# Optimization experiments

Measured on AMD Instinct MI355X. Metric: run time of the kernel, lower is better.

## Reference

```python
import jax, jax.numpy as jnp
import numpy as np

M, N, D = 4, 65536, 256

def setup_inputs() -> dict:
    key = jax.random.key(0)
    k1, k2, k3 = jax.random.split(key, 3)
    x = jax.random.normal(k1, (M, N, D), dtype=jnp.float32)
    # W[i,j] is the (out,in) weight of fusion_layers[i][j]; b[i,j] its bias.
    W = jax.random.normal(k2, (M, M, D, D), dtype=jnp.float32) * (1.0 / np.sqrt(D))
    b = jax.random.normal(k3, (M, M, D), dtype=jnp.float32) * 0.02
    return {"x": x, "W": W, "b": b}

def reference(x, W, b):
    # x: [M, N, D] stacked modality features (zip(*features) rows vectorized over N)
    # out[i] = x[i] + sum_{j != i} (x[j] @ W[i,j]^T + b[i,j])
    m = x.shape[0]
    mask = (1.0 - jnp.eye(m)).astype(x.dtype)            # zero on diagonal (skip i==j)
    y = jnp.einsum('ijef,jnf->ijne', W, x) + b[:, :, None, :]  # [M, M, N, D]
    out = x + jnp.einsum('ij,ijne->ine', mask, y)         # fused masked accumulation
    return out
```

## Files before the change

### kernel.cpp

```cpp
#include <hip/hip_runtime.h>
#include <hip/hip_bf16.h>
#include <stdint.h>

#define NN 65536
#define DD 256

typedef uint32_t u32;
typedef __attribute__((ext_vector_type(4))) float f32x4;
typedef __attribute__((ext_vector_type(4))) u32 u32x4;
typedef __attribute__((ext_vector_type(2))) u32 u32x2;
typedef __attribute__((ext_vector_type(8))) short s16x8;

__device__ inline unsigned short f2bf(float f) {
    union { float f; u32 u; } v; v.f = f;
    u32 u = v.u;
    return (unsigned short)((u + 0x7fffu + ((u >> 16) & 1u)) >> 16);
}

__device__ inline float bf2f(unsigned short h) {
    union { u32 u; float f; } v; v.u = (u32)h << 16;
    return v.f;
}

__device__ inline void gl2lds16(const void* g, void* s) {
    __builtin_amdgcn_global_load_lds(
        (const __attribute__((address_space(1))) void*)g,
        (__attribute__((address_space(3))) void*)s, 16, 0, 0);
}

__global__ void prep_w256(const float* __restrict__ W, unsigned short* __restrict__ Wimg) {
    int t = blockIdx.x * blockDim.x + threadIdx.x;
    int E = t * 4;
    int tile = E >> 14;
    int pin = E & 16383;
    int col = pin >> 6;
    int r2e = pin & 63;
    int ct = tile >> 4;
    int j = (tile >> 2) & 3;
    int kk = tile & 3;
    int kl = r2e ^ ((col & 7) << 3);
    int i = ct;
    int e = col;
    int f = kk * 64 + kl;
    u32 p0, p1;
    if (i == j) {
        p0 = 0u; p1 = 0u;
    } else {
        f32x4 w = *(const f32x4*)(W + ((size_t)((i * 4 + j) * 256 + e) << 8) + f);
        p0 = (u32)f2bf(w[0]) | ((u32)f2bf(w[1]) << 16);
        p1 = (u32)f2bf(w[2]) | ((u32)f2bf(w[3]) << 16);
    }
    u32x2 pr = {p0, p1};
    *(u32x2*)(Wimg + E) = pr;
}

__global__ void prep_w128(const float* __restrict__ W, unsigned short* __restrict__ Wimg) {
    int t = blockIdx.x * blockDim.x + threadIdx.x;
    int E = t * 4;
    int tile = E >> 13;
    int pin = E & 8191;
    int col = pin >> 6;
    int r2e = pin & 63;
    int ct = tile >> 4;
    int j = (tile >> 2) & 3;
    int kk = tile & 3;
    int kl = r2e ^ ((col & 7) << 3);
    int c = ct * 128 + col;
    int i = c >> 8, e = c & 255;
    int f = kk * 64 + kl;
    u32 p0, p1;
    if (i == j) {
        p0 = 0u; p1 = 0u;
    } else {
        f32x4 w = *(const f32x4*)(W + ((size_t)((i * 4 + j) * 256 + e) << 8) + f);
        p0 = (u32)f2bf(w[0]) | ((u32)f2bf(w[1]) << 16);
        p1 = (u32)f2bf(w[2]) | ((u32)f2bf(w[3]) << 16);
    }
    u32x2 pr = {p0, p1};
    *(u32x2*)(Wimg + E) = pr;
}

__global__ void prep_x(const float* __restrict__ x, unsigned short* __restrict__ Ximg) {
    int t = blockIdx.x * blockDim.x + threadIdx.x;
    long long E = (long long)t * 4;
    int tile = (int)(E >> 14);
    int pin = (int)(E & 16383);
    int row = pin >> 6;
    int r2e = pin & 63;
    int kk = tile & 3;
    int rt = (tile >> 2) & 255;
    int j = tile >> 10;
    int kl = r2e ^ ((row & 7) << 3);
    int n = rt * 256 + row;
    int f = kk * 64 + kl;
    f32x4 v = *(const f32x4*)(x + ((size_t)j * NN + n) * DD + f);
    u32 p0 = (u32)f2bf(v[0]) | ((u32)f2bf(v[1]) << 16);
    u32 p1 = (u32)f2bf(v[2]) | ((u32)f2bf(v[3]) << 16);
    u32x2 pr = {p0, p1};
    *(u32x2*)(Ximg + E) = pr;
}

__global__ void prep_b(const float* __restrict__ b, float* __restrict__ bsum) {
    int c = blockIdx.x * blockDim.x + threadIdx.x;
    if (c >= 1024) return;
    int i = c >> 8, e = c & 255;
    float s = 0.0f;
    #pragma unroll
    for (int j = 0; j < 4; ++j)
        if (j != i) s += b[((i * 4 + j) << 8) + e];
    bsum[c] = s;
}

__global__ __launch_bounds__(512, 2) void fusion_gemm14(
    const unsigned short* __restrict__ Wimg, const unsigned short* __restrict__ Ximg,
    const float* __restrict__ bsum, float* __restrict__ out) {
    __shared__ __attribute__((aligned(16))) char lds[2][65536];

    const int tid = threadIdx.x;
    const int bid = blockIdx.x;
    const int xcd = bid & 7;
    const int slot = bid >> 3;
    const int ct = slot & 3;
    const int rhi = slot >> 2;
    const int rtile = rhi * 8 + xcd;
    const int n0 = rtile * 256;
    const int col0 = ct * 256;

    const int lane = tid & 63;
    const int wid = tid >> 6;
    const int wm = wid & 1;
    const int wn = wid >> 1;

    f32x4 acc[8][4];
    #pragma unroll
    for (int a = 0; a < 8; ++a)
        #pragma unroll
        for (int b2 = 0; b2 < 4; ++b2)
            acc[a][b2] = (f32x4){0.f, 0.f, 0.f, 0.f};

    const char* WimgB = (const char*)Wimg;
    const char* XimgB = (const char*)Ximg;
    const u32 loff = (u32)(wid * 1024);
    const u32 goff = (u32)(wid * 1024 + lane * 16);

    s16x8 fA0[2][4], fA1[2][4];
    s16x8 fB0[2][2], fB1[2][2];

#define STAGE_TILE(t_, D_)                                                            \
    {                                                                                 \
        int jj_ = (t_) >> 2;                                                          \
        int j_ = jj_ + (jj_ >= ct);                                                   \
        int kk_ = (t_) & 3;                                                           \
        const char* as_ = XimgB + (((size_t)((j_ * 256 + rtile) * 4 + kk_)) << 15) + goff; \
        const char* bs_ = WimgB + (((size_t)((ct * 4 + j_) * 4 + kk_)) << 15) + goff; \
        _Pragma("unroll")                                                             \
        for (int q = 0; q < 4; ++q) {                                                 \
            gl2lds16(as_ + q * 8192, (D_) + q * 8192 + loff);                         \
            gl2lds16(bs_ + q * 8192, (D_) + 32768 + q * 8192 + loff);                 \
        }                                                                             \
    }

#define RD_A(BUF_, mh_, SET_)                                                         \
    _Pragma("unroll")                                                                 \
    for (int kh = 0; kh < 2; ++kh) {                                                  \
        _Pragma("unroll")                                                             \
        for (int fm = 0; fm < 4; ++fm) {                                              \
            int r_ = wm * 128 + ((mh_) * 4 + fm) * 16 + (lane & 15);                  \
            u32 o_ = (u32)(r_ * 128 + kh * 64 + (lane >> 4) * 16);                    \
            o_ ^= (u32)((r_ & 7) << 4);                                               \
            SET_[kh][fm] = *(const s16x8*)((BUF_) + o_);                              \
        }                                                                             \
    }

#define RD_B(BUF_, nh_, SET_)                                                         \
    _Pragma("unroll")                                                                 \
    for (int kh = 0; kh < 2; ++kh) {                                                  \
        _Pragma("unroll")                                                             \
        for (int fn = 0; fn < 2; ++fn) {                                              \
            int c_ = wn * 64 + ((nh_) * 2 + fn) * 16 + (lane & 15);                   \
            u32 o_ = (u32)(c_ * 128 + kh * 64 + (lane >> 4) * 16);                    \
            o_ ^= (u32)((c_ & 7) << 4);                                               \
            SET_[kh][fn] = *(const s16x8*)((BUF_) + 32768 + o_);                      \
        }                                                                             \
    }

#define MM(AS_, BS_, mh_, nh_)                                                        \
    _Pragma("unroll")                                                                 \
    for (int kh = 0; kh < 2; ++kh) {                                                  \
        _Pragma("unroll")                                                             \
        for (int fm = 0; fm < 4; ++fm) {                                              \
            _Pragma("unroll")                                                         \
            for (int fn = 0; fn < 2; ++fn) {                                          \
                acc[(mh_) * 4 + fm][(nh_) * 2 + fn] =                                 \
                    __builtin_amdgcn_mfma_f32_16x16x32_bf16(                          \
                        AS_[kh][fm], BS_[kh][fn],                                     \
                        acc[(mh_) * 4 + fm][(nh_) * 2 + fn], 0, 0, 0);                \
            }                                                                         \
        }                                                                             \
    }

    STAGE_TILE(0, lds[0]);
    asm volatile("s_waitcnt vmcnt(0)" ::: "memory");
    __builtin_amdgcn_s_barrier();

    #pragma unroll 1
    for (int t = 0; t < 12; ++t) {
        const char* Bf = lds[t & 1];
        char* Of = lds[(t + 1) & 1];

        if (t < 11) STAGE_TILE(t + 1, Of);

        RD_A(Bf, 0, fA0);
        RD_B(Bf, 0, fB0);
        __builtin_amdgcn_s_setprio(1);
        MM(fA0, fB0, 0, 0);
        RD_B(Bf, 1, fB1);
        MM(fA0, fB1, 0, 1);
        RD_A(Bf, 1, fA1);
        MM(fA1, fB1, 1, 1);
        MM(fA1, fB0, 1, 0);
        __builtin_amdgcn_s_setprio(0);

        asm volatile("s_waitcnt vmcnt(0)" ::: "memory");
        __builtin_amdgcn_s_barrier();
    }

#undef STAGE_TILE
#undef RD_A
#undef RD_B
#undef MM

    {
        char* R = (char*)lds;
        #pragma unroll
        for (int kk = 0; kk < 4; ++kk) {
            const char* rs = XimgB + (((size_t)((ct * 256 + rtile) * 4 + kk)) << 15) + goff;
            #pragma unroll
            for (int q = 0; q < 4; ++q)
                gl2lds16(rs + q * 8192, R + kk * 32768 + q * 8192 + loff);
        }
        asm volatile("s_waitcnt vmcnt(0)" ::: "memory");
        __builtin_amdgcn_s_barrier();
    }

    const int r0 = (lane >> 4) * 4;
    const int cl = lane & 15;
    const char* Rb = (const char*)lds + (size_t)wn * 32768;
    #pragma unroll
    for (int mf = 0; mf < 8; ++mf) {
        #pragma unroll
        for (int nf = 0; nf < 4; ++nf) {
            int col_l = wn * 64 + nf * 16 + cl;
            float bs = bsum[col0 + col_l];
            #pragma unroll
            for (int r = 0; r < 4; ++r) {
                int row = wm * 128 + mf * 16 + r0 + r;
                int r2e = (nf * 16 + cl) ^ ((row & 7) << 3);
                float res = bf2f(*(const unsigned short*)(Rb + row * 128 + r2e * 2));
                int n = n0 + row;
                size_t oidx = ((size_t)ct * NN + n) * DD + col_l;
                out[oidx] = acc[mf][nf][r] + res + bs;
            }
        }
    }
}

__global__ __launch_bounds__(256, 2) void fusion_gemm_fb(
    const float* __restrict__ x, const unsigned short* __restrict__ Wimg,
    const float* __restrict__ bsum, float* __restrict__ out) {
    __shared__ __attribute__((aligned(16))) unsigned short Alds[128 * 64];
    __shared__ __attribute__((aligned(16))) unsigned short Blds[2][128 * 64];

    const int tid = threadIdx.x;
    const int bid = blockIdx.x;
    const int xcd = bid & 7;
    const int slot = bid >> 3;
    const int ct = slot & 7;
    const int rhi = slot >> 3;
    const int rtile = rhi * 8 + xcd;
    const int n0 = rtile * 128;
    const int col0 = ct * 128;
    const int i = ct >> 1;

    const int lane = tid & 63;
    const int wid = tid >> 6;
    const int wm = wid >> 1;
    const int wn = wid & 1;

    f32x4 acc[4][4];
    #pragma unroll
    for (int a = 0; a < 4; ++a)
        #pragma unroll
        for (int b2 = 0; b2 < 4; ++b2)
            acc[a][b2] = (f32x4){0.f, 0.f, 0.f, 0.f};

    const int sr = tid >> 1;
    const int sh = tid & 1;
    char* Ab = (char*)Alds;
    const char* WimgB = (const char*)Wimg;

    f32x4 av[8];
    {
        int j0 = (i == 0) ? 1 : 0;
        const float* asrc = x + (size_t)j0 * ((size_t)NN * DD) + (size_t)(n0 + sr) * DD + sh * 32;
        #pragma unroll
        for (int q = 0; q < 8; ++q) av[q] = *(const f32x4*)(asrc + q * 4);
        const char* base = WimgB + (((size_t)(ct * 4 + j0) * 4 + 0) << 14) + wid * 1024 + lane * 16;
        char* lb = (char*)Blds[0] + wid * 1024;
        #pragma unroll
        for (int q = 0; q < 4; ++q) gl2lds16(base + q * 4096, lb + q * 4096);
    }

    for (int t = 0; t < 12; ++t) {
        __syncthreads();
        #pragma unroll
        for (int q = 0; q < 4; ++q) {
            f32x4 v0 = av[2 * q], v1 = av[2 * q + 1];
            u32x4 p;
            p[0] = (u32)f2bf(v0[0]) | ((u32)f2bf(v0[1]) << 16);
            p[1] = (u32)f2bf(v0[2]) | ((u32)f2bf(v0[3]) << 16);
            p[2] = (u32)f2bf(v1[0]) | ((u32)f2bf(v1[1]) << 16);
            p[3] = (u32)f2bf(v1[2]) | ((u32)f2bf(v1[3]) << 16);
            u32 o = (u32)(sr * 128 + sh * 64 + q * 16);
            o ^= (u32)((sr & 7) << 4);
            *(u32x4*)(Ab + o) = p;
        }
        __syncthreads();

        if (t < 11) {
            int tn = t + 1;
            int jjn = tn >> 2;
            int jn = jjn + (jjn >= i);
            int kkn = tn & 3;
            const char* base = WimgB + (((size_t)(ct * 4 + jn) * 4 + kkn) << 14) + wid * 1024 + lane * 16;
            char* lb = (char*)Blds[tn & 1] + wid * 1024;
            #pragma unroll
            for (int q = 0; q < 4; ++q) gl2lds16(base + q * 4096, lb + q * 4096);
            const float* asrc = x + (size_t)jn * ((size_t)NN * DD) + (size_t)(n0 + sr) * DD + kkn * 64 + sh * 32;
            #pragma unroll
            for (int q = 0; q < 8; ++q) av[q] = *(const f32x4*)(asrc + q * 4);
        }

        const char* Bb = (const char*)Blds[t & 1];
        #pragma unroll
        for (int kh = 0; kh < 2; ++kh) {
            s16x8 af[4], bfr[4];
            #pragma unroll
            for (int fm = 0; fm < 4; ++fm) {
                int row = wm * 64 + fm * 16 + (lane & 15);
                u32 o = (u32)(row * 128 + kh * 64 + (lane >> 4) * 16);
                o ^= (u32)((row & 7) << 4);
                af[fm] = *(const s16x8*)(Ab + o);
            }
            #pragma unroll
            for (int fn = 0; fn < 4; ++fn) {
                int col = wn * 64 + fn * 16 + (lane & 15);
                u32 o = (u32)(col * 128 + kh * 64 + (lane >> 4) * 16);
                o ^= (u32)((col & 7) << 4);
                bfr[fn] = *(const s16x8*)(Bb + o);
            }
            #pragma unroll
            for (int fm = 0; fm < 4; ++fm)
                #pragma unroll
                for (int fn = 0; fn < 4; ++fn)
                    acc[fm][fn] = __builtin_amdgcn_mfma_f32_16x16x32_bf16(
                        af[fm], bfr[fn], acc[fm][fn], 0, 0, 0);
        }
    }

    const int r0 = (lane >> 4) * 4;
    const int cl = lane & 15;
    #pragma unroll
    for (int fm = 0; fm < 4; ++fm) {
        #pragma unroll
        for (int fn = 0; fn < 4; ++fn) {
            int col_l = wn * 64 + fn * 16 + cl;
            int cglob = col0 + col_l;
            float bs = bsum[cglob];
            int e = cglob & 255;
            #pragma unroll
            for (int r = 0; r < 4; ++r) {
                int row_l = wm * 64 + fm * 16 + r0 + r;
                int n = n0 + row_l;
                size_t oidx = ((size_t)i * NN + n) * DD + e;
                out[oidx] = acc[fm][fn][r] + x[oidx] + bs;
            }
        }
    }
}

extern "C" void kernel_launch(void* const* d_in, const int* in_sizes, int n_in,
                              void* d_out, int out_size, void* d_ws, size_t ws_size,
                              hipStream_t stream) {
    const float* x = (const float*)d_in[0];
    const float* W = (const float*)d_in[1];
    const float* b = (const float*)d_in[2];
    float* out = (float*)d_out;

    unsigned short* Wimg = (unsigned short*)d_ws;
    float* bsum = (float*)((char*)d_ws + ((size_t)8 << 20));
    const size_t ximg_off = (size_t)9 << 20;
    const size_t need = ximg_off + ((size_t)128 << 20);

    if (ws_size >= need) {
        unsigned short* Ximg = (unsigned short*)((char*)d_ws + ximg_off);
        hipLaunchKernelGGL(prep_b, dim3(4), dim3(256), 0, stream, b, bsum);
        hipLaunchKernelGGL(prep_w256, dim3(1024), dim3(256), 0, stream, W, Wimg);
        hipLaunchKernelGGL(prep_x, dim3(65536), dim3(256), 0, stream, x, Ximg);
        hipLaunchKernelGGL(fusion_gemm14, dim3(1024), dim3(512), 0, stream, Wimg, Ximg, bsum, out);
    } else {
        float* bsum2 = (float*)((char*)d_ws + ((size_t)2 << 20));
        hipLaunchKernelGGL(prep_b, dim3(4), dim3(256), 0, stream, b, bsum2);
        hipLaunchKernelGGL(prep_w128, dim3(1024), dim3(256), 0, stream, W, Wimg);
        hipLaunchKernelGGL(fusion_gemm_fb, dim3(4096), dim3(256), 0, stream, x, Wimg, bsum2, out);
    }
}
```

Baseline: 223.7 us.

## Drop X prepass; use producer/consumer warps converting fp32 X to bf16 in-kernel

Removes the separate prep_x pass that wrote a 128MB bf16 image of x. The main GEMM kernel now splits its warps: four producer warps load fp32 x, convert it to bf16 into swizzled LDS, and DMA weight tiles, while four consumer warps run the MFMA work. Output tiles shrink to 128 columns, so the grid doubles. The bias and weight prep kernels are merged into one launch. The aim is to cut global memory traffic and launch overhead, at the cost of halving the warps doing math and re-reading x for each column tile.

New measurement: 389.6 us. 74.2% more time.

```diff
diff --git a/kernel.cpp b/kernel.cpp
--- a/kernel.cpp
+++ b/kernel.cpp
@@ -28,108 +28,68 @@
         (__attribute__((address_space(3))) void*)s, 16, 0, 0);
 }
 
-__global__ void prep_w256(const float* __restrict__ W, unsigned short* __restrict__ Wimg) {
-    int t = blockIdx.x * blockDim.x + threadIdx.x;
-    int E = t * 4;
-    int tile = E >> 14;
-    int pin = E & 16383;
-    int col = pin >> 6;
-    int r2e = pin & 63;
-    int ct = tile >> 4;
-    int j = (tile >> 2) & 3;
-    int kk = tile & 3;
-    int kl = r2e ^ ((col & 7) << 3);
-    int i = ct;
-    int e = col;
-    int f = kk * 64 + kl;
-    u32 p0, p1;
-    if (i == j) {
-        p0 = 0u; p1 = 0u;
+__global__ void prep_small(const float* __restrict__ W, const float* __restrict__ b,
+                           unsigned short* __restrict__ Wimg, float* __restrict__ bsum) {
+    int bid = blockIdx.x;
+    if (bid < 1024) {
+        int t = bid * 256 + threadIdx.x;
+        int E = t * 4;
+        int tile = E >> 13;
+        int pin = E & 8191;
+        int col = pin >> 6;
+        int r2e = pin & 63;
+        int ct = tile >> 4;
+        int j = (tile >> 2) & 3;
+        int kk = tile & 3;
+        int kl = r2e ^ ((col & 7) << 3);
+        int c = ct * 128 + col;
+        int i = c >> 8, e = c & 255;
+        int f = kk * 64 + kl;
+        u32 p0, p1;
+        if (i == j) {
+            p0 = 0u; p1 = 0u;
+        } else {
+            f32x4 w = *(const f32x4*)(W + ((size_t)((i * 4 + j) * 256 + e) << 8) + f);
+            p0 = (u32)f2bf(w[0]) | ((u32)f2bf(w[1]) << 16);
+            p1 = (u32)f2bf(w[2]) | ((u32)f2bf(w[3]) << 16);
+        }
+        u32x2 pr = {p0, p1};
+        *(u32x2*)(Wimg + E) = pr;
     } else {
-        f32x4 w = *(const f32x4*)(W + ((size_t)((i * 4 + j) * 256 + e) << 8) + f);
-        p0 = (u32)f2bf(w[0]) | ((u32)f2bf(w[1]) << 16);
-        p1 = (u32)f2bf(w[2]) | ((u32)f2bf(w[3]) << 16);
-    }
-    u32x2 pr = {p0, p1};
-    *(u32x2*)(Wimg + E) = pr;
-}
-
-__global__ void prep_w128(const float* __restrict__ W, unsigned short* __restrict__ Wimg) {
-    int t = blockIdx.x * blockDim.x + threadIdx.x;
-    int E = t * 4;
-    int tile = E >> 13;
-    int pin = E & 8191;
-    int col = pin >> 6;
-    int r2e = pin & 63;
-    int ct = tile >> 4;
-    int j = (tile >> 2) & 3;
-    int kk = tile & 3;
-    int kl = r2e ^ ((col & 7) << 3);
-    int c = ct * 128 + col;
-    int i = c >> 8, e = c & 255;
-    int f = kk * 64 + kl;
-    u32 p0, p1;
-    if (i == j) {
-        p0 = 0u; p1 = 0u;
-    } else {
-        f32x4 w = *(const f32x4*)(W + ((size_t)((i * 4 + j) * 256 + e) << 8) + f);
-        p0 = (u32)f2bf(w[0]) | ((u32)f2bf(w[1]) << 16);
-        p1 = (u32)f2bf(w[2]) | ((u32)f2bf(w[3]) << 16);
-    }
-    u32x2 pr = {p0, p1};
-    *(u32x2*)(Wimg + E) = pr;
-}
-
-__global__ void prep_x(const float* __restrict__ x, unsigned short* __restrict__ Ximg) {
-    int t = blockIdx.x * blockDim.x + threadIdx.x;
-    long long E = (long long)t * 4;
-    int tile = (int)(E >> 14);
-    int pin = (int)(E & 16383);
-    int row = pin >> 6;
-    int r2e = pin & 63;
-    int kk = tile & 3;
-    int rt = (tile >> 2) & 255;
-    int j = tile >> 10;
-    int kl = r2e ^ ((row & 7) << 3);
-    int n = rt * 256 + row;
-    int f = kk * 64 + kl;
-    f32x4 v = *(const f32x4*)(x + ((size_t)j * NN + n) * DD + f);
-    u32 p0 = (u32)f2bf(v[0]) | ((u32)f2bf(v[1]) << 16);
-    u32 p1 = (u32)f2bf(v[2]) | ((u32)f2bf(v[3]) << 16);
-    u32x2 pr = {p0, p1};
-    *(u32x2*)(Ximg + E) = pr;
-}
-
-__global__ void prep_b(const float* __restrict__ b, float* __restrict__ bsum) {
-    int c = blockIdx.x * blockDim.x + threadIdx.x;
-    if (c >= 1024) return;
-    int i = c >> 8, e = c & 255;
-    float s = 0.0f;
-    #pragma unroll
-    for (int j = 0; j < 4; ++j)
-        if (j != i) s += b[((i * 4 + j) << 8) + e];
-    bsum[c] = s;
-}
-
-__global__ __launch_bounds__(512, 2) void fusion_gemm14(
-    const unsigned short* __restrict__ Wimg, const unsigned short* __restrict__ Ximg,
+        int c = (bid - 1024) * 256 + threadIdx.x;
+        if (c < 1024) {
+            int i = c >> 8, e = c & 255;
+            float s = 0.0f;
+            #pragma unroll
+            for (int j = 0; j < 4; ++j)
+                if (j != i) s += b[((i * 4 + j) << 8) + e];
+            bsum[c] = s;
+        }
+    }
+}
+
+__global__ __launch_bounds__(512, 2) void fusion_gemm17(
+    const float* __restrict__ x, const unsigned short* __restrict__ Wimg,
     const float* __restrict__ bsum, float* __restrict__ out) {
-    __shared__ __attribute__((aligned(16))) char lds[2][65536];
+    __shared__ __attribute__((aligned(16))) char lds[2][49152];
 
     const int tid = threadIdx.x;
     const int bid = blockIdx.x;
     const int xcd = bid & 7;
     const int slot = bid >> 3;
-    const int ct = slot & 3;
-    const int rhi = slot >> 2;
+    const int ct = slot & 7;
+    const int rhi = slot >> 3;
     const int rtile = rhi * 8 + xcd;
     const int n0 = rtile * 256;
-    const int col0 = ct * 256;
+    const int i = ct >> 1;
 
     const int lane = tid & 63;
     const int wid = tid >> 6;
+    const bool consumer = (wid < 4);
     const int wm = wid & 1;
-    const int wn = wid >> 1;
+    const int wn = (wid >> 1) & 1;
+    const int p = tid - 256;
+    const int pw = wid - 4;
 
     f32x4 acc[8][4];
     #pragma unroll
@@ -139,24 +99,39 @@
             acc[a][b2] = (f32x4){0.f, 0.f, 0.f, 0.f};
 
     const char* WimgB = (const char*)Wimg;
-    const char* XimgB = (const char*)Ximg;
-    const u32 loff = (u32)(wid * 1024);
-    const u32 goff = (u32)(wid * 1024 + lane * 16);
-
     s16x8 fA0[2][4], fA1[2][4];
     s16x8 fB0[2][2], fB1[2][2];
 
-#define STAGE_TILE(t_, D_)                                                            \
+#define P_LOAD(j_, kk_)                                                               \
     {                                                                                 \
-        int jj_ = (t_) >> 2;                                                          \
-        int j_ = jj_ + (jj_ >= ct);                                                   \
-        int kk_ = (t_) & 3;                                                           \
-        const char* as_ = XimgB + (((size_t)((j_ * 256 + rtile) * 4 + kk_)) << 15) + goff; \
-        const char* bs_ = WimgB + (((size_t)((ct * 4 + j_) * 4 + kk_)) << 15) + goff; \
-        _Pragma("unroll")                                                             \
-        for (int q = 0; q < 4; ++q) {                                                 \
-            gl2lds16(as_ + q * 8192, (D_) + q * 8192 + loff);                         \
-            gl2lds16(bs_ + q * 8192, (D_) + 32768 + q * 8192 + loff);                 \
+        const float* as_ = x + (size_t)(j_) * ((size_t)NN * DD)                       \
+                           + (size_t)(n0 + p) * DD + (kk_) * 64;                      \
+        _Pragma("unroll")                                                             \
+        for (int q = 0; q < 16; ++q) av[q] = *(const f32x4*)(as_ + q * 4);            \
+    }
+
+#define P_BDMA(j_, kk_, D_)                                                           \
+    {                                                                                 \
+        const char* bs_ = WimgB + (((size_t)((ct * 4 + (j_)) * 4 + (kk_))) << 14)     \
+                          + pw * 4096 + lane * 16;                                    \
+        _Pragma("unroll")                                                             \
+        for (int q = 0; q < 4; ++q)                                                   \
+            gl2lds16(bs_ + q * 1024, (D_) + 32768 + pw * 4096 + q * 1024);            \
+    }
+
+#define P_WRITE_A(D_)                                                                 \
+    {                                                                                 \
+        _Pragma("unroll")                                                             \
+        for (int q = 0; q < 8; ++q) {                                                 \
+            f32x4 v0 = av[2 * q], v1 = av[2 * q + 1];                                 \
+            u32x4 pk;                                                                 \
+            pk[0] = (u32)f2bf(v0[0]) | ((u32)f2bf(v0[1]) << 16);                      \
+            pk[1] = (u32)f2bf(v0[2]) | ((u32)f2bf(v0[3]) << 16);                      \
+            pk[2] = (u32)f2bf(v1[0]) | ((u32)f2bf(v1[1]) << 16);                      \
+            pk[3] = (u32)f2bf(v1[2]) | ((u32)f2bf(v1[3]) << 16);                      \
+            u32 o_ = (u32)(p * 128 + q * 16);                                         \
+            o_ ^= (u32)((p & 7) << 4);                                                \
+            *(u32x4*)((D_) + o_) = pk;                                                \
         }                                                                             \
     }
 
@@ -199,67 +174,91 @@
         }                                                                             \
     }
 
-    STAGE_TILE(0, lds[0]);
+    if (!consumer) {
+        f32x4 av[16];
+        int jj = 0, j0 = jj + (jj >= i);
+        P_LOAD(j0, 0);
+        P_BDMA(j0, 0, (char*)lds[0]);
+        P_WRITE_A((char*)lds[0]);
+    }
+    asm volatile("s_waitcnt lgkmcnt(0)" ::: "memory");
     asm volatile("s_waitcnt vmcnt(0)" ::: "memory");
     __builtin_amdgcn_s_barrier();
+    __builtin_amdgcn_sched_barrier(0);
 
     #pragma unroll 1
     for (int t = 0; t < 12; ++t) {
         const char* Bf = lds[t & 1];
         char* Of = lds[(t + 1) & 1];
 
-        if (t < 11) STAGE_TILE(t + 1, Of);
-
-        RD_A(Bf, 0, fA0);
-        RD_B(Bf, 0, fB0);
-        __builtin_amdgcn_s_setprio(1);
-        MM(fA0, fB0, 0, 0);
-        RD_B(Bf, 1, fB1);
-        MM(fA0, fB1, 0, 1);
-        RD_A(Bf, 1, fA1);
-        MM(fA1, fB1, 1, 1);
-        MM(fA1, fB0, 1, 0);
-        __builtin_amdgcn_s_setprio(0);
-
+        if (consumer) {
+            RD_A(Bf, 0, fA0);
+            RD_B(Bf, 0, fB0);
+            __builtin_amdgcn_s_setprio(1);
+            MM(fA0, fB0, 0, 0);
+            RD_B(Bf, 1, fB1);
+            MM(fA0, fB1, 0, 1);
+            RD_A(Bf, 1, fA1);
+            MM(fA1, fB1, 1, 1);
+            MM(fA1, fB0, 1, 0);
+            __builtin_amdgcn_s_setprio(0);
+        } else if (t < 11) {
+            f32x4 av[16];
+            int jj = (t + 1) >> 2;
+            int jn = jj + (jj >= i);
+            int kkn = (t + 1) & 3;
+            P_LOAD(jn, kkn);
+            P_BDMA(jn, kkn, Of);
+            P_WRITE_A(Of);
+        }
+
+        asm volatile("s_waitcnt lgkmcnt(0)" ::: "memory");
         asm volatile("s_waitcnt vmcnt(0)" ::: "memory");
         __builtin_amdgcn_s_barrier();
-    }
-
-#undef STAGE_TILE
+        __builtin_amdgcn_sched_barrier(0);
+    }
+
+    if (!consumer) {
+        #pragma unroll
+        for (int h = 0; h < 2; ++h) {
+            f32x4 av[16];
+            int kkr = (ct & 1) * 2 + h;
+            P_LOAD(i, kkr);
+            P_WRITE_A((char*)lds[h]);
+        }
+    }
+    asm volatile("s_waitcnt lgkmcnt(0)" ::: "memory");
+    asm volatile("s_waitcnt vmcnt(0)" ::: "memory");
+    __builtin_amdgcn_s_barrier();
+    __builtin_amdgcn_sched_barrier(0);
+
+#undef P_LOAD
+#undef P_BDMA
+#undef P_WRITE_A
 #undef RD_A
 #undef RD_B
 #undef MM
 
-    {
-        char* R = (char*)lds;
-        #pragma unroll
-        for (int kk = 0; kk < 4; ++kk) {
-            const char* rs = XimgB + (((size_t)((ct * 256 + rtile) * 4 + kk)) << 15) + goff;
-            #pragma unroll
-            for (int q = 0; q < 4; ++q)
-                gl2lds16(rs + q * 8192, R + kk * 32768 + q * 8192 + loff);
-        }
-        asm volatile("s_waitcnt vmcnt(0)" ::: "memory");
-        __builtin_amdgcn_s_barrier();
-    }
-
-    const int r0 = (lane >> 4) * 4;
-    const int cl = lane & 15;
-    const char* Rb = (const char*)lds + (size_t)wn * 32768;
-    #pragma unroll
-    for (int mf = 0; mf < 8; ++mf) {
-        #pragma unroll
-        for (int nf = 0; nf < 4; ++nf) {
-            int col_l = wn * 64 + nf * 16 + cl;
-            float bs = bsum[col0 + col_l];
-            #pragma unroll
-            for (int r = 0; r < 4; ++r) {
-                int row = wm * 128 + mf * 16 + r0 + r;
-                int r2e = (nf * 16 + cl) ^ ((row & 7) << 3);
-                float res = bf2f(*(const unsigned short*)(Rb + row * 128 + r2e * 2));
-                int n = n0 + row;
-                size_t oidx = ((size_t)ct * NN + n) * DD + col_l;
-                out[oidx] = acc[mf][nf][r] + res + bs;
+    if (consumer) {
+        const int r0 = (lane >> 4) * 4;
+        const int cl = lane & 15;
+        const char* Rb = (const char*)lds[wn];
+        #pragma unroll
+        for (int mf = 0; mf < 8; ++mf) {
+            #pragma unroll
+            for (int nf = 0; nf < 4; ++nf) {
+                int col_l = wn * 64 + nf * 16 + cl;
+                int e = (ct & 1) * 128 + col_l;
+                float bs = bsum[i * 256 + e];
+                #pragma unroll
+                for (int r = 0; r < 4; ++r) {
+                    int row = wm * 128 + mf * 16 + r0 + r;
+                    int r2e = (nf * 16 + cl) ^ ((row & 7) << 3);
+                    float res = bf2f(*(const unsigned short*)(Rb + row * 128 + r2e * 2));
+                    int n = n0 + row;
+                    size_t oidx = ((size_t)i * NN + n) * DD + e;
+                    out[oidx] = acc[mf][nf][r] + res + bs;
+                }
             }
         }
     }
@@ -316,14 +315,14 @@
         #pragma unroll
         for (int q = 0; q < 4; ++q) {
             f32x4 v0 = av[2 * q], v1 = av[2 * q + 1];
-            u32x4 p;
-            p[0] = (u32)f2bf(v0[0]) | ((u32)f2bf(v0[1]) << 16);
-            p[1] = (u32)f2bf(v0[2]) | ((u32)f2bf(v0[3]) << 16);
-            p[2] = (u32)f2bf(v1[0]) | ((u32)f2bf(v1[1]) << 16);
-            p[3] = (u32)f2bf(v1[2]) | ((u32)f2bf(v1[3]) << 16);
+            u32x4 pk;
+            pk[0] = (u32)f2bf(v0[0]) | ((u32)f2bf(v0[1]) << 16);
+            pk[1] = (u32)f2bf(v0[2]) | ((u32)f2bf(v0[3]) << 16);
+            pk[2] = (u32)f2bf(v1[0]) | ((u32)f2bf(v1[1]) << 16);
+            pk[3] = (u32)f2bf(v1[2]) | ((u32)f2bf(v1[3]) << 16);
             u32 o = (u32)(sr * 128 + sh * 64 + q * 16);
             o ^= (u32)((sr & 7) << 4);
-            *(u32x4*)(Ab + o) = p;
+            *(u32x4*)(Ab + o) = pk;
         }
         __syncthreads();
 
@@ -398,20 +397,14 @@
     float* out = (float*)d_out;
 
     unsigned short* Wimg = (unsigned short*)d_ws;
-    float* bsum = (float*)((char*)d_ws + ((size_t)8 << 20));
-    const size_t ximg_off = (size_t)9 << 20;
-    const size_t need = ximg_off + ((size_t)128 << 20);
+    float* bsum = (float*)((char*)d_ws + ((size_t)2 << 20));
+    const size_t need = ((size_t)2 << 20) + 4096;
+
+    hipLaunchKernelGGL(prep_small, dim3(1028), dim3(256), 0, stream, W, b, Wimg, bsum);
 
     if (ws_size >= need) {
-        unsigned short* Ximg = (unsigned short*)((char*)d_ws + ximg_off);
-        hipLaunchKernelGGL(prep_b, dim3(4), dim3(256), 0, stream, b, bsum);
-        hipLaunchKernelGGL(prep_w256, dim3(1024), dim3(256), 0, stream, W, Wimg);
-        hipLaunchKernelGGL(prep_x, dim3(65536), dim3(256), 0, stream, x, Ximg);
-        hipLaunchKernelGGL(fusion_gemm14, dim3(1024), dim3(512), 0, stream, Wimg, Ximg, bsum, out);
+        hipLaunchKernelGGL(fusion_gemm17, dim3(2048), dim3(512), 0, stream, x, Wimg, bsum, out);
     } else {
-        float* bsum2 = (float*)((char*)d_ws + ((size_t)2 << 20));
-        hipLaunchKernelGGL(prep_b, dim3(4), dim3(256), 0, stream, b, bsum2);
-        hipLaunchKernelGGL(prep_w128, dim3(1024), dim3(256), 0, stream, W, Wimg);
-        hipLaunchKernelGGL(fusion_gemm_fb, dim3(4096), dim3(256), 0, stream, x, Wimg, bsum2, out);
-    }
-}
+        hipLaunchKernelGGL(fusion_gemm_fb, dim3(4096), dim3(256), 0, stream, x, Wimg, bsum, out);
+    }
+}
```
